# Optimization experiments

Measured on AMD Instinct MI355X. Metric: run time of the kernel, lower is better.

Reference implementation:

```python
import jax, jax.numpy as jnp
import numpy as np
import math

B, H, LQ, LK, D = 2, 16, 2048, 2048, 128

def setup_inputs() -> dict:
    key = jax.random.key(0)
    kq, kk, kv, km = jax.random.split(key, 4)
    return {
        "query": jax.random.normal(kq, (B, H, LQ, D), dtype=jnp.float32),
        "key": jax.random.normal(kk, (B, H, LK, D), dtype=jnp.float32),
        "value": jax.random.normal(kv, (B, H, LK, D), dtype=jnp.float32),
        # positive integer multiplicities in [1, 8] so log() is finite
        "key_multiplicities": jax.random.randint(km, (B, LK), 1, 9, dtype=jnp.int32),
    }

def reference(query, key, value, key_multiplicities):
    scale = 1.0 / math.sqrt(query.shape[-1])
    # scores: [B, H, Lq, Lk]
    scores = jnp.einsum("bhqd,bhkd->bhqk", query, key) * scale
    # additive log-multiplicity bias, broadcast over heads and queries
    log_mult = jnp.log(key_multiplicities.astype(scores.dtype))  # [B, Lk]
    scores = scores + log_mult[:, None, None, :]
    attn = jax.nn.softmax(scores, axis=-1)
    # dropout_p = 0.0 -> identity
    return jnp.einsum("bhqk,bhkd->bhqd", attn, value)
```

## Files before the change

kernel.cpp:

```cpp
#include <hip/hip_runtime.h>
#include <hip/hip_bf16.h>

constexpr int B_  = 2;
constexpr int H_  = 16;
constexpr int LQ_ = 2048;
constexpr int LK_ = 2048;
constexpr int D_  = 128;

constexpr int BM = 128;
constexpr int BN = 64;
constexpr int NT = LK_ / BN;
constexpr int TILE_SH = 64 * 128;

constexpr float SCALE_LOG2E = 0.12751649734586414f;

typedef short s16x4 __attribute__((ext_vector_type(4)));
typedef short s16x8 __attribute__((ext_vector_type(8)));
typedef float f32x4 __attribute__((ext_vector_type(4)));

#define MFMA16 __builtin_amdgcn_mfma_f32_16x16x32_bf16

#if __has_builtin(__builtin_amdgcn_exp2f)
#define EXP2(x) __builtin_amdgcn_exp2f(x)
#else
#define EXP2(x) exp2f(x)
#endif
#if __has_builtin(__builtin_amdgcn_logf)
#define LOG2(x) __builtin_amdgcn_logf(x)
#else
#define LOG2(x) log2f(x)
#endif

static __device__ __forceinline__ int pk2bf(float a, float b) {
  float2 t{a, b};
  __hip_bfloat162 h = __float22bfloat162_rn(t);
  return *reinterpret_cast<int*>(&h);
}

static __device__ __forceinline__ void dma16(const short* g, short* l) {
  __builtin_amdgcn_global_load_lds(
      (const __attribute__((address_space(1))) void*)g,
      (__attribute__((address_space(3))) void*)l, 16, 0, 0);
}

__global__ __launch_bounds__(256)
void prep(const float* __restrict__ kg, const float* __restrict__ vg,
          const int* __restrict__ multg, short* __restrict__ wsK,
          short* __restrict__ wsV, float* __restrict__ wsBias) {
  __shared__ float tileF[64 * 133];
  const int tid = threadIdx.x;
  const int wg  = blockIdx.x;
  const float* kp = kg + (size_t)wg * 64 * 128;
  const float* vp = vg + (size_t)wg * 64 * 128;
  short* wk = wsK + (size_t)wg * TILE_SH;
  short* wv = wsV + (size_t)wg * TILE_SH;

#pragma unroll
  for (int i = 0; i < 4; ++i) {
    int idx = tid + i * 256;
    int row = idx >> 4, blk = idx & 15;
    const float* src = kp + row * 128 + blk * 8;
    float4 a = *(const float4*)src;
    float4 c4 = *(const float4*)(src + 4);
    int4 t;
    t.x = pk2bf(a.x, a.y);  t.y = pk2bf(a.z, a.w);
    t.z = pk2bf(c4.x, c4.y); t.w = pk2bf(c4.z, c4.w);
    int pos = blk ^ (row & 15);
    *(int4*)&wk[row * 128 + pos * 8] = t;
  }

#pragma unroll
  for (int i = 0; i < 8; ++i) {
    int idx = tid + i * 256;
    int key = idx >> 5, d0 = (idx & 31) * 4;
    float4 a = *(const float4*)(vp + key * 128 + d0);
    float* dst = &tileF[key * 133 + d0];
    dst[0] = a.x; dst[1] = a.y; dst[2] = a.z; dst[3] = a.w;
  }
  __syncthreads();
#pragma unroll
  for (int i = 0; i < 4; ++i) {
    int idx = tid + i * 256;
    int d = idx >> 3, kgrp = idx & 7;
    float v[8];
#pragma unroll
    for (int j = 0; j < 8; ++j) v[j] = tileF[(kgrp * 8 + j) * 133 + d];
    int4 t;
    t.x = pk2bf(v[0], v[1]); t.y = pk2bf(v[2], v[3]);
    t.z = pk2bf(v[4], v[5]); t.w = pk2bf(v[6], v[7]);
    int pos = kgrp ^ ((d >> 1) & 7);
    *(int4*)&wv[d * 64 + pos * 8] = t;
  }

  if (wg < 8) {
    int b = wg >> 2;
    for (int j = tid; j < 512; j += 256) {
      int i0 = (wg & 3) * 512 + j;
      wsBias[b * LK_ + i0] = LOG2((float)multg[b * LK_ + i0]);
    }
  }
}

__global__ __launch_bounds__(256, 2)
void attn_fwd(const float* __restrict__ qg, const short* __restrict__ wsK,
              const short* __restrict__ wsV, const float* __restrict__ wsBias,
              float* __restrict__ outg) {
  __shared__ alignas(16) short Kbuf[2][TILE_SH];
  __shared__ alignas(16) short Vbuf[2][TILE_SH];
  __shared__ alignas(16) short Psh[128 * 64];

  const int tid  = threadIdx.x;
  const int w    = tid >> 6;
  const int lane = tid & 63;
  const int c    = lane & 15;
  const int qd   = lane >> 4;

  const int L   = blockIdx.y * gridDim.x + blockIdx.x;
  const int k8  = L >> 3;
  const int qb  = k8 & 15;
  const int bh  = (L & 7) * 4 + (k8 >> 4);
  const int b   = bh >> 4;

  const float* qptr = qg + (size_t)bh * LQ_ * D_;
  float*       optr = outg + (size_t)bh * LQ_ * D_;
  const short* kws  = wsK + (size_t)bh * NT * TILE_SH;
  const short* vws  = wsV + (size_t)bh * NT * TILE_SH;
  const float* bias = wsBias + b * LK_;

  const int q0 = qb * BM + w * 32;
  s16x8 qf[2][4];
#pragma unroll
  for (int qs = 0; qs < 2; ++qs) {
    const float* qrow = qptr + (size_t)(q0 + qs * 16 + c) * D_ + qd * 8;
#pragma unroll
    for (int kf = 0; kf < 4; ++kf) {
      float4 a  = *(const float4*)(qrow + kf * 32);
      float4 bq = *(const float4*)(qrow + kf * 32 + 4);
      int4 t;
      t.x = pk2bf(a.x * SCALE_LOG2E, a.y * SCALE_LOG2E);
      t.y = pk2bf(a.z * SCALE_LOG2E, a.w * SCALE_LOG2E);
      t.z = pk2bf(bq.x * SCALE_LOG2E, bq.y * SCALE_LOG2E);
      t.w = pk2bf(bq.z * SCALE_LOG2E, bq.w * SCALE_LOG2E);
      qf[qs][kf] = *(s16x8*)&t;
    }
  }

  f32x4 o[2][8];
  float m_r[2], l_r[2];
#pragma unroll
  for (int qs = 0; qs < 2; ++qs) {
#pragma unroll
    for (int dt = 0; dt < 8; ++dt) o[qs][dt] = (f32x4){0.f, 0.f, 0.f, 0.f};
    m_r[qs] = -INFINITY; l_r[qs] = 0.f;
  }

  auto dmaKV = [&](int kt, int bb) {
    const short* gK = kws + (size_t)kt * TILE_SH;
    const short* gV = vws + (size_t)kt * TILE_SH;
#pragma unroll
    for (int i = 0; i < 4; ++i) {
      int off = (w * 4 + i) * 512;
      dma16(gK + off + lane * 8, &Kbuf[bb][off]);
      dma16(gV + off + lane * 8, &Vbuf[bb][off]);
    }
  };

  dmaKV(0, 0);
  __syncthreads();

  for (int kt = 0; kt < NT; ++kt) {
    const int cur = kt & 1;
    if (kt + 1 < NT) dmaKV(kt + 1, cur ^ 1);

    float bvf[4][4];
#pragma unroll
    for (int ct = 0; ct < 4; ++ct) {
      float4 bv = *(const float4*)&bias[kt * BN + ct * 16 + qd * 4];
      bvf[ct][0] = bv.x; bvf[ct][1] = bv.y; bvf[ct][2] = bv.z; bvf[ct][3] = bv.w;
    }

    f32x4 St[2][4];
#pragma unroll
    for (int qs = 0; qs < 2; ++qs)
#pragma unroll
      for (int ct = 0; ct < 4; ++ct) St[qs][ct] = (f32x4){0.f, 0.f, 0.f, 0.f};

#pragma unroll
    for (int ct = 0; ct < 4; ++ct) {
      const short* kb = &Kbuf[cur][(ct * 16 + c) * 128];
#pragma unroll
      for (int kf = 0; kf < 4; ++kf) {
        s16x8 kfr = *(const s16x8*)&kb[((kf * 4 + qd) ^ c) * 8];
        St[0][ct] = MFMA16(kfr, qf[0][kf], St[0][ct], 0, 0, 0);
        St[1][ct] = MFMA16(kfr, qf[1][kf], St[1][ct], 0, 0, 0);
      }
    }

#pragma unroll
    for (int qs = 0; qs < 2; ++qs) {
      float x[4][4];
#pragma unroll
      for (int ct = 0; ct < 4; ++ct)
#pragma unroll
        for (int reg = 0; reg < 4; ++reg)
          x[ct][reg] = St[qs][ct][reg] + bvf[ct][reg];

      float mx = x[0][0];
#pragma unroll
      for (int ct = 0; ct < 4; ++ct)
#pragma unroll
        for (int reg = 0; reg < 4; ++reg) mx = fmaxf(mx, x[ct][reg]);
      mx = fmaxf(mx, __shfl_xor(mx, 16));
      mx = fmaxf(mx, __shfl_xor(mx, 32));

      float mn    = fmaxf(m_r[qs], mx);
      float alpha = EXP2(m_r[qs] - mn);
      m_r[qs] = mn;

      float rs = 0.f;
#pragma unroll
      for (int ct = 0; ct < 4; ++ct)
#pragma unroll
        for (int reg = 0; reg < 4; ++reg) {
          float p = EXP2(x[ct][reg] - mn);
          x[ct][reg] = p;
          rs += p;
        }
      rs += __shfl_xor(rs, 16);
      rs += __shfl_xor(rs, 32);
      l_r[qs] = l_r[qs] * alpha + rs;

      const int pr = w * 32 + qs * 16 + c;
#pragma unroll
      for (int ct = 0; ct < 4; ++ct) {
        int2 pk;
        pk.x = pk2bf(x[ct][0], x[ct][1]);
        pk.y = pk2bf(x[ct][2], x[ct][3]);
        int pos = (ct * 2 + (qd >> 1)) ^ (pr & 7);
        *(int2*)&Psh[pr * 64 + pos * 8 + (qd & 1) * 4] = pk;
      }

      float ar[4];
#pragma unroll
      for (int reg = 0; reg < 4; ++reg) ar[reg] = __shfl(alpha, qd * 4 + reg);
#pragma unroll
      for (int dt = 0; dt < 8; ++dt)
#pragma unroll
        for (int reg = 0; reg < 4; ++reg) o[qs][dt][reg] *= ar[reg];
    }

    s16x8 pf[2][2];
#pragma unroll
    for (int qs = 0; qs < 2; ++qs) {
      const int pr = w * 32 + qs * 16 + c;
#pragma unroll
      for (int kf = 0; kf < 2; ++kf) {
        int pos = (kf * 4 + qd) ^ (pr & 7);
        pf[qs][kf] = *(const s16x8*)&Psh[pr * 64 + pos * 8];
      }
    }
#pragma unroll
    for (int dt = 0; dt < 8; ++dt) {
      int d = dt * 16 + c;
      const short* vb = &Vbuf[cur][d * 64];
      s16x8 vf[2];
#pragma unroll
      for (int kf = 0; kf < 2; ++kf)
        vf[kf] = *(const s16x8*)&vb[((kf * 4 + qd) ^ ((d >> 1) & 7)) * 8];
#pragma unroll
      for (int qs = 0; qs < 2; ++qs)
#pragma unroll
        for (int kf = 0; kf < 2; ++kf)
          o[qs][dt] = MFMA16(pf[qs][kf], vf[kf], o[qs][dt], 0, 0, 0);
    }

    __syncthreads();
  }

#pragma unroll
  for (int qs = 0; qs < 2; ++qs) {
    float lr[4];
#pragma unroll
    for (int reg = 0; reg < 4; ++reg) lr[reg] = __shfl(l_r[qs], qd * 4 + reg);
#pragma unroll
    for (int reg = 0; reg < 4; ++reg) {
      float inv = 1.0f / lr[reg];
      int row = q0 + qs * 16 + qd * 4 + reg;
      float* orow = optr + (size_t)row * D_ + c;
#pragma unroll
      for (int dt = 0; dt < 8; ++dt) orow[dt * 16] = o[qs][dt][reg] * inv;
    }
  }
}

extern "C" void kernel_launch(void* const* d_in, const int* in_sizes, int n_in,
                              void* d_out, int out_size, void* d_ws, size_t ws_size,
                              hipStream_t stream) {
  const float* q = (const float*)d_in[0];
  const float* k = (const float*)d_in[1];
  const float* v = (const float*)d_in[2];
  const int* mult = (const int*)d_in[3];
  float* out = (float*)d_out;

  constexpr size_t KV_BYTES = (size_t)B_ * H_ * LK_ * D_ * 2;
  short* wsK = (short*)d_ws;
  short* wsV = (short*)((char*)d_ws + KV_BYTES);
  float* wsBias = (float*)((char*)d_ws + 2 * KV_BYTES);

  prep<<<dim3(B_ * H_ * NT), dim3(256), 0, stream>>>(k, v, mult, wsK, wsV, wsBias);

  dim3 grid(LQ_ / BM, B_ * H_);
  attn_fwd<<<grid, dim3(256), 0, stream>>>(q, wsK, wsV, wsBias, out);
}
```

Measured before the change: 231.5 us.

## Split key range across two workgroups with 32-key tiles and merge partials

Adds a split-K flash attention path. Each (batch, head, query block) is handled by two workgroups, each covering half the keys with 32-key tiles and smaller LDS so four workgroups can share a CU. The partial outputs and running max/sum are written to workspace, and a separate merge kernel combines them. The goal is a grid of 1024 workgroups instead of 512 for better occupancy on the CUs. The cost is an extra launch plus a full fp32 partial-output write and re-read. The new path runs only when the workspace is large enough; otherwise the old path is kept.

```diff
diff --git a/kernel.cpp b/kernel.cpp
--- a/kernel.cpp
+++ b/kernel.cpp
@@ -8,10 +8,6 @@
 constexpr int D_  = 128;
 
 constexpr int BM = 128;
-constexpr int BN = 64;
-constexpr int NT = LK_ / BN;
-constexpr int TILE_SH = 64 * 128;
-
 constexpr float SCALE_LOG2E = 0.12751649734586414f;
 
 typedef short s16x4 __attribute__((ext_vector_type(4)));
@@ -43,17 +39,276 @@
       (__attribute__((address_space(3))) void*)l, 16, 0, 0);
 }
 
+constexpr int TILE32 = 32 * 128;
+
 __global__ __launch_bounds__(256)
-void prep(const float* __restrict__ kg, const float* __restrict__ vg,
-          const int* __restrict__ multg, short* __restrict__ wsK,
-          short* __restrict__ wsV, float* __restrict__ wsBias) {
+void prep32(const float* __restrict__ kg, const float* __restrict__ vg,
+            const int* __restrict__ multg, short* __restrict__ wsK,
+            short* __restrict__ wsV, float* __restrict__ wsBias) {
   __shared__ float tileF[64 * 133];
   const int tid = threadIdx.x;
   const int wg  = blockIdx.x;
   const float* kp = kg + (size_t)wg * 64 * 128;
   const float* vp = vg + (size_t)wg * 64 * 128;
-  short* wk = wsK + (size_t)wg * TILE_SH;
-  short* wv = wsV + (size_t)wg * TILE_SH;
+  short* wk = wsK + (size_t)wg * 2 * TILE32;
+  short* wv = wsV + (size_t)wg * 2 * TILE32;
+
+#pragma unroll
+  for (int i = 0; i < 4; ++i) {
+    int idx = tid + i * 256;
+    int row = idx >> 4, blk = idx & 15;
+    const float* src = kp + row * 128 + blk * 8;
+    float4 a = *(const float4*)src;
+    float4 c4 = *(const float4*)(src + 4);
+    int4 t;
+    t.x = pk2bf(a.x, a.y);  t.y = pk2bf(a.z, a.w);
+    t.z = pk2bf(c4.x, c4.y); t.w = pk2bf(c4.z, c4.w);
+    int pos = blk ^ (row & 15);
+    *(int4*)&wk[(row >> 5) * TILE32 + (row & 31) * 128 + pos * 8] = t;
+  }
+
+#pragma unroll
+  for (int i = 0; i < 8; ++i) {
+    int idx = tid + i * 256;
+    int key = idx >> 5, d0 = (idx & 31) * 4;
+    float4 a = *(const float4*)(vp + key * 128 + d0);
+    float* dst = &tileF[key * 133 + d0];
+    dst[0] = a.x; dst[1] = a.y; dst[2] = a.z; dst[3] = a.w;
+  }
+  __syncthreads();
+#pragma unroll
+  for (int i = 0; i < 4; ++i) {
+    int idx = tid + i * 256;
+    int d = idx >> 3, kgrp = idx & 7;
+    float v[8];
+#pragma unroll
+    for (int j = 0; j < 8; ++j) v[j] = tileF[(kgrp * 8 + j) * 133 + d];
+    int4 t;
+    t.x = pk2bf(v[0], v[1]); t.y = pk2bf(v[2], v[3]);
+    t.z = pk2bf(v[4], v[5]); t.w = pk2bf(v[6], v[7]);
+    int pos = (kgrp & 3) ^ ((d >> 1) & 3);
+    *(int4*)&wv[(kgrp >> 2) * TILE32 + d * 32 + pos * 8] = t;
+  }
+
+  if (wg < 8) {
+    int b = wg >> 2;
+    for (int j = tid; j < 512; j += 256) {
+      int i0 = (wg & 3) * 512 + j;
+      wsBias[b * LK_ + i0] = LOG2((float)multg[b * LK_ + i0]);
+    }
+  }
+}
+
+__global__ __launch_bounds__(256, 4)
+void attn32(const float* __restrict__ qg, const short* __restrict__ wsK,
+            const short* __restrict__ wsV, const float* __restrict__ wsBias,
+            float* __restrict__ outg, float* __restrict__ part1,
+            float2* __restrict__ wsML) {
+  __shared__ alignas(16) short Kbuf[2][TILE32];
+  __shared__ alignas(16) short Vbuf[2][TILE32];
+  __shared__ alignas(16) short Psh[128 * 32];
+
+  const int tid  = threadIdx.x;
+  const int w    = tid >> 6;
+  const int lane = tid & 63;
+  const int c    = lane & 15;
+  const int qd   = lane >> 4;
+
+  const int L   = blockIdx.x;
+  const int xcd = L & 7;
+  const int idx = L >> 3;
+  const int bh  = xcd * 4 + (idx >> 5);
+  const int rem = idx & 31;
+  const int qb  = rem & 15;
+  const int s   = rem >> 4;
+  const int b   = bh >> 4;
+
+  const float* qptr = qg + (size_t)bh * LQ_ * D_;
+  float* obase = (s ? part1 : outg) + (size_t)bh * LQ_ * D_;
+  const short* kws = wsK + ((size_t)bh * 64 + s * 32) * TILE32;
+  const short* vws = wsV + ((size_t)bh * 64 + s * 32) * TILE32;
+  const float* bias = wsBias + b * LK_ + s * 1024;
+  float2* mlp = wsML + (size_t)s * 32 * LQ_ + (size_t)bh * LQ_;
+
+  const int q0 = qb * BM + w * 32;
+  s16x8 qf[2][4];
+#pragma unroll
+  for (int qs = 0; qs < 2; ++qs) {
+    const float* qrow = qptr + (size_t)(q0 + qs * 16 + c) * D_ + qd * 8;
+#pragma unroll
+    for (int kf = 0; kf < 4; ++kf) {
+      float4 a  = *(const float4*)(qrow + kf * 32);
+      float4 bq = *(const float4*)(qrow + kf * 32 + 4);
+      int4 t;
+      t.x = pk2bf(a.x * SCALE_LOG2E, a.y * SCALE_LOG2E);
+      t.y = pk2bf(a.z * SCALE_LOG2E, a.w * SCALE_LOG2E);
+      t.z = pk2bf(bq.x * SCALE_LOG2E, bq.y * SCALE_LOG2E);
+      t.w = pk2bf(bq.z * SCALE_LOG2E, bq.w * SCALE_LOG2E);
+      qf[qs][kf] = *(s16x8*)&t;
+    }
+  }
+
+  f32x4 o[2][8];
+  float m_r[2], l_r[2];
+#pragma unroll
+  for (int qs = 0; qs < 2; ++qs) {
+#pragma unroll
+    for (int dt = 0; dt < 8; ++dt) o[qs][dt] = (f32x4){0.f, 0.f, 0.f, 0.f};
+    m_r[qs] = -INFINITY; l_r[qs] = 0.f;
+  }
+
+  auto dmaKV = [&](int kt, int bb) {
+    const short* gK = kws + (size_t)kt * TILE32;
+    const short* gV = vws + (size_t)kt * TILE32;
+#pragma unroll
+    for (int i = 0; i < 2; ++i) {
+      int off = (w * 2 + i) * 512;
+      dma16(gK + off + lane * 8, &Kbuf[bb][off]);
+      dma16(gV + off + lane * 8, &Vbuf[bb][off]);
+    }
+  };
+
+  dmaKV(0, 0);
+  __syncthreads();
+
+  for (int kt = 0; kt < 32; ++kt) {
+    const int cur = kt & 1;
+    if (kt + 1 < 32) dmaKV(kt + 1, cur ^ 1);
+
+    float bvf[2][4];
+#pragma unroll
+    for (int ct = 0; ct < 2; ++ct) {
+      float4 bv = *(const float4*)&bias[kt * 32 + ct * 16 + qd * 4];
+      bvf[ct][0] = bv.x; bvf[ct][1] = bv.y; bvf[ct][2] = bv.z; bvf[ct][3] = bv.w;
+    }
+
+    f32x4 St[2][2];
+#pragma unroll
+    for (int qs = 0; qs < 2; ++qs)
+#pragma unroll
+      for (int ct = 0; ct < 2; ++ct) St[qs][ct] = (f32x4){0.f, 0.f, 0.f, 0.f};
+
+#pragma unroll
+    for (int ct = 0; ct < 2; ++ct) {
+      const short* kb = &Kbuf[cur][(ct * 16 + c) * 128];
+#pragma unroll
+      for (int kf = 0; kf < 4; ++kf) {
+        s16x8 kfr = *(const s16x8*)&kb[((kf * 4 + qd) ^ c) * 8];
+        St[0][ct] = MFMA16(kfr, qf[0][kf], St[0][ct], 0, 0, 0);
+        St[1][ct] = MFMA16(kfr, qf[1][kf], St[1][ct], 0, 0, 0);
+      }
+    }
+
+#pragma unroll
+    for (int qs = 0; qs < 2; ++qs) {
+      float x[2][4];
+#pragma unroll
+      for (int ct = 0; ct < 2; ++ct)
+#pragma unroll
+        for (int reg = 0; reg < 4; ++reg)
+          x[ct][reg] = St[qs][ct][reg] + bvf[ct][reg];
+
+      float mx = x[0][0];
+#pragma unroll
+      for (int ct = 0; ct < 2; ++ct)
+#pragma unroll
+        for (int reg = 0; reg < 4; ++reg) mx = fmaxf(mx, x[ct][reg]);
+      mx = fmaxf(mx, __shfl_xor(mx, 16));
+      mx = fmaxf(mx, __shfl_xor(mx, 32));
+
+      float mn    = fmaxf(m_r[qs], mx);
+      float alpha = EXP2(m_r[qs] - mn);
+      m_r[qs] = mn;
+
+      float rs = 0.f;
+#pragma unroll
+      for (int ct = 0; ct < 2; ++ct)
+#pragma unroll
+        for (int reg = 0; reg < 4; ++reg) {
+          float p = EXP2(x[ct][reg] - mn);
+          x[ct][reg] = p;
+          rs += p;
+        }
+      rs += __shfl_xor(rs, 16);
+      rs += __shfl_xor(rs, 32);
+      l_r[qs] = l_r[qs] * alpha + rs;
+
+      const int pr = w * 32 + qs * 16 + c;
+#pragma unroll
+      for (int ct = 0; ct < 2; ++ct) {
+        int2 pk;
+        pk.x = pk2bf(x[ct][0], x[ct][1]);
+        pk.y = pk2bf(x[ct][2], x[ct][3]);
+        int pos = (ct * 2 + (qd >> 1)) ^ (pr & 3);
+        *(int2*)&Psh[pr * 32 + pos * 8 + (qd & 1) * 4] = pk;
+      }
+
+#pragma unroll
+      for (int dt = 0; dt < 8; ++dt)
+#pragma unroll
+        for (int reg = 0; reg < 4; ++reg) o[qs][dt][reg] *= alpha;
+    }
+
+    s16x8 pf[2];
+#pragma unroll
+    for (int qs = 0; qs < 2; ++qs) {
+      const int pr = w * 32 + qs * 16 + c;
+      pf[qs] = *(const s16x8*)&Psh[pr * 32 + (qd ^ (pr & 3)) * 8];
+    }
+#pragma unroll
+    for (int dt = 0; dt < 8; ++dt) {
+      int d = dt * 16 + c;
+      s16x8 vf = *(const s16x8*)&Vbuf[cur][d * 32 + (qd ^ ((d >> 1) & 3)) * 8];
+      o[0][dt] = MFMA16(vf, pf[0], o[0][dt], 0, 0, 0);
+      o[1][dt] = MFMA16(vf, pf[1], o[1][dt], 0, 0, 0);
+    }
+
+    __syncthreads();
+  }
+
+#pragma unroll
+  for (int qs = 0; qs < 2; ++qs) {
+    float* orow = obase + (size_t)(q0 + qs * 16 + c) * D_ + qd * 4;
+#pragma unroll
+    for (int dt = 0; dt < 8; ++dt)
+      *(f32x4*)(orow + dt * 16) = o[qs][dt];
+    if (qd == 0)
+      mlp[q0 + qs * 16 + c] = make_float2(m_r[qs], l_r[qs]);
+  }
+}
+
+__global__ __launch_bounds__(256)
+void merge(float4* __restrict__ out, const float4* __restrict__ p1,
+           const float2* __restrict__ ml0, const float2* __restrict__ ml1) {
+  int gid = blockIdx.x * 256 + threadIdx.x;
+  int row = gid >> 5;
+  float2 a = ml0[row], bb = ml1[row];
+  float m = fmaxf(a.x, bb.x);
+  float s0 = EXP2(a.x - m), s1 = EXP2(bb.x - m);
+  float inv = 1.0f / (a.y * s0 + bb.y * s1);
+  float4 o0 = out[gid], o1 = p1[gid];
+  float4 r;
+  r.x = (o0.x * s0 + o1.x * s1) * inv;
+  r.y = (o0.y * s0 + o1.y * s1) * inv;
+  r.z = (o0.z * s0 + o1.z * s1) * inv;
+  r.w = (o0.w * s0 + o1.w * s1) * inv;
+  out[gid] = r;
+}
+
+constexpr int NT64 = 32;
+constexpr int TILE64 = 64 * 128;
+
+__global__ __launch_bounds__(256)
+void prep64(const float* __restrict__ kg, const float* __restrict__ vg,
+            const int* __restrict__ multg, short* __restrict__ wsK,
+            short* __restrict__ wsV, float* __restrict__ wsBias) {
+  __shared__ float tileF[64 * 133];
+  const int tid = threadIdx.x;
+  const int wg  = blockIdx.x;
+  const float* kp = kg + (size_t)wg * 64 * 128;
+  const float* vp = vg + (size_t)wg * 64 * 128;
+  short* wk = wsK + (size_t)wg * TILE64;
+  short* wv = wsV + (size_t)wg * TILE64;
 
 #pragma unroll
   for (int i = 0; i < 4; ++i) {
@@ -68,7 +323,6 @@
     int pos = blk ^ (row & 15);
     *(int4*)&wk[row * 128 + pos * 8] = t;
   }
-
 #pragma unroll
   for (int i = 0; i < 8; ++i) {
     int idx = tid + i * 256;
@@ -91,7 +345,6 @@
     int pos = kgrp ^ ((d >> 1) & 7);
     *(int4*)&wv[d * 64 + pos * 8] = t;
   }
-
   if (wg < 8) {
     int b = wg >> 2;
     for (int j = tid; j < 512; j += 256) {
@@ -102,11 +355,11 @@
 }
 
 __global__ __launch_bounds__(256, 2)
-void attn_fwd(const float* __restrict__ qg, const short* __restrict__ wsK,
-              const short* __restrict__ wsV, const float* __restrict__ wsBias,
-              float* __restrict__ outg) {
-  __shared__ alignas(16) short Kbuf[2][TILE_SH];
-  __shared__ alignas(16) short Vbuf[2][TILE_SH];
+void attn64(const float* __restrict__ qg, const short* __restrict__ wsK,
+            const short* __restrict__ wsV, const float* __restrict__ wsBias,
+            float* __restrict__ outg) {
+  __shared__ alignas(16) short Kbuf[2][TILE64];
+  __shared__ alignas(16) short Vbuf[2][TILE64];
   __shared__ alignas(16) short Psh[128 * 64];
 
   const int tid  = threadIdx.x;
@@ -123,8 +376,8 @@
 
   const float* qptr = qg + (size_t)bh * LQ_ * D_;
   float*       optr = outg + (size_t)bh * LQ_ * D_;
-  const short* kws  = wsK + (size_t)bh * NT * TILE_SH;
-  const short* vws  = wsV + (size_t)bh * NT * TILE_SH;
+  const short* kws  = wsK + (size_t)bh * NT64 * TILE64;
+  const short* vws  = wsV + (size_t)bh * NT64 * TILE64;
   const float* bias = wsBias + b * LK_;
 
   const int q0 = qb * BM + w * 32;
@@ -155,8 +408,8 @@
   }
 
   auto dmaKV = [&](int kt, int bb) {
-    const short* gK = kws + (size_t)kt * TILE_SH;
-    const short* gV = vws + (size_t)kt * TILE_SH;
+    const short* gK = kws + (size_t)kt * TILE64;
+    const short* gV = vws + (size_t)kt * TILE64;
 #pragma unroll
     for (int i = 0; i < 4; ++i) {
       int off = (w * 4 + i) * 512;
@@ -168,14 +421,14 @@
   dmaKV(0, 0);
   __syncthreads();
 
-  for (int kt = 0; kt < NT; ++kt) {
+  for (int kt = 0; kt < NT64; ++kt) {
     const int cur = kt & 1;
-    if (kt + 1 < NT) dmaKV(kt + 1, cur ^ 1);
+    if (kt + 1 < NT64) dmaKV(kt + 1, cur ^ 1);
 
     float bvf[4][4];
 #pragma unroll
     for (int ct = 0; ct < 4; ++ct) {
-      float4 bv = *(const float4*)&bias[kt * BN + ct * 16 + qd * 4];
+      float4 bv = *(const float4*)&bias[kt * 64 + ct * 16 + qd * 4];
       bvf[ct][0] = bv.x; bvf[ct][1] = bv.y; bvf[ct][2] = bv.z; bvf[ct][3] = bv.w;
     }
 
@@ -302,13 +555,30 @@
   const int* mult = (const int*)d_in[3];
   float* out = (float*)d_out;
 
-  constexpr size_t KV_BYTES = (size_t)B_ * H_ * LK_ * D_ * 2;
-  short* wsK = (short*)d_ws;
-  short* wsV = (short*)((char*)d_ws + KV_BYTES);
-  float* wsBias = (float*)((char*)d_ws + 2 * KV_BYTES);
-
-  prep<<<dim3(B_ * H_ * NT), dim3(256), 0, stream>>>(k, v, mult, wsK, wsV, wsBias);
-
-  dim3 grid(LQ_ / BM, B_ * H_);
-  attn_fwd<<<grid, dim3(256), 0, stream>>>(q, wsK, wsV, wsBias, out);
-}
+  constexpr size_t KV_BYTES  = (size_t)B_ * H_ * LK_ * D_ * 2;
+  constexpr size_t O_BYTES   = (size_t)B_ * H_ * LQ_ * D_ * 4;
+  constexpr size_t ML_BYTES  = (size_t)2 * B_ * H_ * LQ_ * 8;
+  constexpr size_t NEED_NEW  = 2 * KV_BYTES + O_BYTES + ML_BYTES + LK_ * B_ * 4;
+
+  if (ws_size >= NEED_NEW) {
+    short*  wsK    = (short*)d_ws;
+    short*  wsV    = (short*)((char*)d_ws + KV_BYTES);
+    float*  part1  = (float*)((char*)d_ws + 2 * KV_BYTES);
+    float2* wsML   = (float2*)((char*)d_ws + 2 * KV_BYTES + O_BYTES);
+    float*  wsBias = (float*)((char*)d_ws + 2 * KV_BYTES + O_BYTES + ML_BYTES);
+    const float2* ml0 = wsML;
+    const float2* ml1 = wsML + (size_t)B_ * H_ * LQ_;
+
+    prep32<<<dim3(B_ * H_ * 32), dim3(256), 0, stream>>>(k, v, mult, wsK, wsV, wsBias);
+    attn32<<<dim3(1024), dim3(256), 0, stream>>>(q, wsK, wsV, wsBias, out, part1, wsML);
+    merge<<<dim3((B_ * H_ * LQ_ * D_ / 4) / 256), dim3(256), 0, stream>>>(
+        (float4*)out, (const float4*)part1, ml0, ml1);
+  } else {
+    short* wsK = (short*)d_ws;
+    short* wsV = (short*)((char*)d_ws + KV_BYTES);
+    float* wsBias = (float*)((char*)d_ws + 2 * KV_BYTES);
+    prep64<<<dim3(B_ * H_ * NT64), dim3(256), 0, stream>>>(k, v, mult, wsK, wsV, wsBias);
+    dim3 grid(LQ_ / BM, B_ * H_);
+    attn64<<<grid, dim3(256), 0, stream>>>(q, wsK, wsV, wsBias, out);
+  }
+}
```

After: 474.1 us. 2.05x slower.
